# Performance work log

Measured on AMD Instinct MI355X. Metric: run time of the kernel, lower is better.

## Reference

```python
import jax, jax.numpy as jnp
import numpy as np

N, C, G, R = 500000, 256, 1024, 16


def setup_inputs() -> dict:
    key = jax.random.key(0)
    k1, k2, k3, k4 = jax.random.split(key, 4)
    x = jax.random.normal(k1, (N, C), dtype=jnp.float32)
    batch_idx = jnp.sort(jax.random.randint(k2, (N,), 0, G))
    # torch Linear weights: W1 [C//R, C], W2 [C, C//R] (no bias)
    W1 = jax.random.normal(k3, (C // R, C), dtype=jnp.float32) / np.sqrt(C)
    W2 = jax.random.normal(k4, (C, C // R), dtype=jnp.float32) / np.sqrt(C // R)
    prelu_a = jnp.asarray(0.25, dtype=jnp.float32)  # nn.PReLU default single param
    return {"x": x, "batch_idx": batch_idx, "num_graphs": G,
            "W1": W1, "prelu_a": prelu_a, "W2": W2}


def reference(x, batch_idx, num_graphs, W1, prelu_a, W2):
    # scatter_mean over graphs: [G, C]
    seg_sum = jax.ops.segment_sum(x, batch_idx, num_segments=num_graphs)
    cnt = jax.ops.segment_sum(jnp.ones((x.shape[0],), x.dtype), batch_idx,
                              num_segments=num_graphs)
    x_mean = seg_sum / jnp.maximum(cnt, 1.0)[:, None]
    # SE bottleneck MLP: Linear -> PReLU -> Linear -> Sigmoid
    h = jnp.einsum('gc,rc->gr', x_mean, W1)          # [G, C//R]
    h = jnp.where(h >= 0, h, prelu_a * h)            # PReLU (scalar a)
    score = jax.nn.sigmoid(jnp.einsum('gr,cr->gc', h, W2))  # [G, C]
    # gather-broadcast multiply back to nodes
    return x * score[batch_idx]
```

## Files before the change

kernel.cpp:

```cpp
#include <hip/hip_runtime.h>

#define CC 256
#define GG 1024
#define RR 16
#define ROWS_PER_BLOCK 256

__global__ void seg_sum_kernel(const float* __restrict__ x,
                               const int* __restrict__ batch_idx,
                               float* __restrict__ seg,
                               float* __restrict__ cnt,
                               int n) {
    const int wave = threadIdx.x >> 6;
    const int lane = threadIdx.x & 63;
    const int base = blockIdx.x * ROWS_PER_BLOCK;
    const int rend = min(base + ROWS_PER_BLOCK, n);

    float4 acc = make_float4(0.f, 0.f, 0.f, 0.f);
    int cur_g = -1;
    int cl = 0;

    for (int row = base + wave; row < rend; row += 4) {
        const int g = batch_idx[row];
        if (g != cur_g) {
            if (cur_g >= 0) {
                float* p = seg + (size_t)cur_g * CC + lane * 4;
                atomicAdd(p + 0, acc.x);
                atomicAdd(p + 1, acc.y);
                atomicAdd(p + 2, acc.z);
                atomicAdd(p + 3, acc.w);
                if (lane == 0) atomicAdd(cnt + cur_g, (float)cl);
            }
            cur_g = g;
            acc = make_float4(0.f, 0.f, 0.f, 0.f);
            cl = 0;
        }
        const float4 v =
            *reinterpret_cast<const float4*>(x + (size_t)row * CC + lane * 4);
        acc.x += v.x; acc.y += v.y; acc.z += v.z; acc.w += v.w;
        ++cl;
    }
    if (cur_g >= 0) {
        float* p = seg + (size_t)cur_g * CC + lane * 4;
        atomicAdd(p + 0, acc.x);
        atomicAdd(p + 1, acc.y);
        atomicAdd(p + 2, acc.z);
        atomicAdd(p + 3, acc.w);
        if (lane == 0) atomicAdd(cnt + cur_g, (float)cl);
    }
}

__global__ void mlp_kernel(const float* __restrict__ seg,
                           const float* __restrict__ cnt,
                           const float* __restrict__ W1,
                           const float* __restrict__ prelu_a,
                           const float* __restrict__ W2,
                           float* __restrict__ score) {
    __shared__ float xm[CC];
    __shared__ float h[RR];
    const int g = blockIdx.x;
    const int t = threadIdx.x;

    const float c   = cnt[g];
    const float inv = 1.0f / fmaxf(c, 1.0f);
    xm[t] = seg[(size_t)g * CC + t] * inv;
    __syncthreads();

    if (t < RR) {
        const float a = *prelu_a;
        float acc = 0.f;
        const float* w = W1 + t * CC;
        #pragma unroll 8
        for (int cc2 = 0; cc2 < CC; ++cc2) acc += xm[cc2] * w[cc2];
        h[t] = (acc >= 0.f) ? acc : a * acc;
    }
    __syncthreads();

    float acc2 = 0.f;
    const float* w2 = W2 + t * RR;
    #pragma unroll
    for (int r = 0; r < RR; ++r) acc2 += h[r] * w2[r];
    score[(size_t)g * CC + t] = 1.0f / (1.0f + __expf(-acc2));
}

__global__ void apply_kernel(const float4* __restrict__ x4,
                             const int* __restrict__ batch_idx,
                             const float4* __restrict__ score4,
                             float4* __restrict__ out4,
                             long total) {
    const long i = (long)blockIdx.x * blockDim.x + threadIdx.x;
    if (i >= total) return;
    const int row = (int)(i >> 6);
    const int c4  = (int)(i & 63);
    const int g   = batch_idx[row];
    const float4 v = x4[i];
    const float4 s = score4[(size_t)g * 64 + c4];
    out4[i] = make_float4(v.x * s.x, v.y * s.y, v.z * s.z, v.w * s.w);
}

extern "C" void kernel_launch(void* const* d_in, const int* in_sizes, int n_in,
                              void* d_out, int out_size, void* d_ws, size_t ws_size,
                              hipStream_t stream) {
    const float* x    = (const float*)d_in[0];
    const int*   bidx = (const int*)d_in[1];
    const float* W1   = (const float*)d_in[3];
    const float* pa   = (const float*)d_in[4];
    const float* W2   = (const float*)d_in[5];
    float*       out  = (float*)d_out;

    const int n = in_sizes[1];

    float* seg   = (float*)d_ws;
    float* cnt   = seg + (size_t)GG * CC;
    float* score = cnt + GG;

    hipMemsetAsync(d_ws, 0, ((size_t)GG * CC + GG) * sizeof(float), stream);

    const int nb1 = (n + ROWS_PER_BLOCK - 1) / ROWS_PER_BLOCK;
    seg_sum_kernel<<<nb1, 256, 0, stream>>>(x, bidx, seg, cnt, n);

    mlp_kernel<<<GG, CC, 0, stream>>>(seg, cnt, W1, pa, W2, score);

    const long total = (long)n * (CC / 4);
    const int nb3 = (int)((total + 255) / 256);
    apply_kernel<<<nb3, 256, 0, stream>>>((const float4*)x, bidx,
                                          (const float4*)score, (float4*)out,
                                          total);
}
```

Baseline: 934.5 us.

## Fuse segment mean, SE MLP and scaling into one per-graph kernel

Replaces the atomic segment-sum, MLP and apply kernels with a binary-search bounds kernel plus one fused kernel where each 1024-thread block owns whole graphs. The block reduces the graph's rows in shared memory, computes the MLP score locally, then re-reads the rows to write the scaled output with nontemporal stores. This removes the memset, the atomics, the per-element batch_idx gather and the score round-trip through global memory. In exchange x is read twice inside one block, possibly hitting cache, and only 256 blocks iterate over 1024 graphs, so uneven graph sizes can leave some blocks working longer than others.

```diff
diff --git a/kernel.cpp b/kernel.cpp
--- a/kernel.cpp
+++ b/kernel.cpp
@@ -3,98 +3,103 @@
 #define CC 256
 #define GG 1024
 #define RR 16
-#define ROWS_PER_BLOCK 256
+#define NB 256
+#define NT_THREADS 1024
 
-__global__ void seg_sum_kernel(const float* __restrict__ x,
-                               const int* __restrict__ batch_idx,
-                               float* __restrict__ seg,
-                               float* __restrict__ cnt,
-                               int n) {
-    const int wave = threadIdx.x >> 6;
-    const int lane = threadIdx.x & 63;
-    const int base = blockIdx.x * ROWS_PER_BLOCK;
-    const int rend = min(base + ROWS_PER_BLOCK, n);
+typedef float f32x4 __attribute__((ext_vector_type(4)));
 
-    float4 acc = make_float4(0.f, 0.f, 0.f, 0.f);
-    int cur_g = -1;
-    int cl = 0;
-
-    for (int row = base + wave; row < rend; row += 4) {
-        const int g = batch_idx[row];
-        if (g != cur_g) {
-            if (cur_g >= 0) {
-                float* p = seg + (size_t)cur_g * CC + lane * 4;
-                atomicAdd(p + 0, acc.x);
-                atomicAdd(p + 1, acc.y);
-                atomicAdd(p + 2, acc.z);
-                atomicAdd(p + 3, acc.w);
-                if (lane == 0) atomicAdd(cnt + cur_g, (float)cl);
-            }
-            cur_g = g;
-            acc = make_float4(0.f, 0.f, 0.f, 0.f);
-            cl = 0;
-        }
-        const float4 v =
-            *reinterpret_cast<const float4*>(x + (size_t)row * CC + lane * 4);
-        acc.x += v.x; acc.y += v.y; acc.z += v.z; acc.w += v.w;
-        ++cl;
+__global__ void bounds_kernel(const int* __restrict__ bidx,
+                              int* __restrict__ bounds, int n) {
+    const int g = blockIdx.x * blockDim.x + threadIdx.x;
+    if (g > GG) return;
+    int lo = 0, hi = n;
+    while (lo < hi) {
+        const int mid = (lo + hi) >> 1;
+        if (bidx[mid] < g) lo = mid + 1; else hi = mid;
     }
-    if (cur_g >= 0) {
-        float* p = seg + (size_t)cur_g * CC + lane * 4;
-        atomicAdd(p + 0, acc.x);
-        atomicAdd(p + 1, acc.y);
-        atomicAdd(p + 2, acc.z);
-        atomicAdd(p + 3, acc.w);
-        if (lane == 0) atomicAdd(cnt + cur_g, (float)cl);
-    }
+    bounds[g] = lo;
 }
 
-__global__ void mlp_kernel(const float* __restrict__ seg,
-                           const float* __restrict__ cnt,
-                           const float* __restrict__ W1,
-                           const float* __restrict__ prelu_a,
-                           const float* __restrict__ W2,
-                           float* __restrict__ score) {
+__global__ __launch_bounds__(NT_THREADS) void fused_kernel(
+        const float* __restrict__ x,
+        const int* __restrict__ bounds,
+        const float* __restrict__ W1,
+        const float* __restrict__ prelu_a,
+        const float* __restrict__ W2,
+        float* __restrict__ out) {
+    __shared__ f32x4 part[16][64];
     __shared__ float xm[CC];
     __shared__ float h[RR];
-    const int g = blockIdx.x;
-    const int t = threadIdx.x;
+    __shared__ float score[CC];
 
-    const float c   = cnt[g];
-    const float inv = 1.0f / fmaxf(c, 1.0f);
-    xm[t] = seg[(size_t)g * CC + t] * inv;
-    __syncthreads();
+    const int t    = threadIdx.x;
+    const int w    = t >> 6;
+    const int lane = t & 63;
 
-    if (t < RR) {
-        const float a = *prelu_a;
-        float acc = 0.f;
-        const float* w = W1 + t * CC;
-        #pragma unroll 8
-        for (int cc2 = 0; cc2 < CC; ++cc2) acc += xm[cc2] * w[cc2];
-        h[t] = (acc >= 0.f) ? acc : a * acc;
+    for (int g = blockIdx.x; g < GG; g += gridDim.x) {
+        const int start = bounds[g];
+        const int end   = bounds[g + 1];
+        const int rows  = end - start;
+        if (rows == 0) continue;
+
+        f32x4 acc = {0.f, 0.f, 0.f, 0.f};
+        #pragma unroll 2
+        for (int r = start + w; r < end; r += 16) {
+            const f32x4 v = *reinterpret_cast<const f32x4*>(
+                x + (size_t)r * CC + 4 * lane);
+            acc += v;
+        }
+        part[w][lane] = acc;
+        __syncthreads();
+        if (w < 8) { part[w][lane] += part[w + 8][lane]; } __syncthreads();
+        if (w < 4) { part[w][lane] += part[w + 4][lane]; } __syncthreads();
+        if (w < 2) { part[w][lane] += part[w + 2][lane]; } __syncthreads();
+        if (w == 0) {
+            const float inv = 1.0f / (float)rows;
+            f32x4 s = part[0][lane] + part[1][lane];
+            s *= inv;
+            reinterpret_cast<f32x4*>(xm)[lane] = s;
+        }
+        __syncthreads();
+
+        if (t < 256) {
+            const int r  = t >> 4;
+            const int sl = t & 15;
+            const float* wrow = W1 + r * CC;
+            float p = 0.f;
+            #pragma unroll
+            for (int c = sl; c < CC; c += 16) p += xm[c] * wrow[c];
+            p += __shfl_xor(p, 1);
+            p += __shfl_xor(p, 2);
+            p += __shfl_xor(p, 4);
+            p += __shfl_xor(p, 8);
+            if (sl == 0) {
+                const float a = *prelu_a;
+                h[r] = (p >= 0.f) ? p : a * p;
+            }
+        }
+        __syncthreads();
+
+        if (t < 256) {
+            const float* w2 = W2 + t * RR;
+            float acc2 = 0.f;
+            #pragma unroll
+            for (int r = 0; r < RR; ++r) acc2 += h[r] * w2[r];
+            score[t] = 1.0f / (1.0f + __expf(-acc2));
+        }
+        __syncthreads();
+
+        const f32x4 sv = reinterpret_cast<const f32x4*>(score)[lane];
+        #pragma unroll 2
+        for (int r = start + w; r < end; r += 16) {
+            const f32x4 v = *reinterpret_cast<const f32x4*>(
+                x + (size_t)r * CC + 4 * lane);
+            const f32x4 o = v * sv;
+            __builtin_nontemporal_store(
+                o, reinterpret_cast<f32x4*>(out + (size_t)r * CC + 4 * lane));
+        }
+        __syncthreads();
     }
-    __syncthreads();
-
-    float acc2 = 0.f;
-    const float* w2 = W2 + t * RR;
-    #pragma unroll
-    for (int r = 0; r < RR; ++r) acc2 += h[r] * w2[r];
-    score[(size_t)g * CC + t] = 1.0f / (1.0f + __expf(-acc2));
-}
-
-__global__ void apply_kernel(const float4* __restrict__ x4,
-                             const int* __restrict__ batch_idx,
-                             const float4* __restrict__ score4,
-                             float4* __restrict__ out4,
-                             long total) {
-    const long i = (long)blockIdx.x * blockDim.x + threadIdx.x;
-    if (i >= total) return;
-    const int row = (int)(i >> 6);
-    const int c4  = (int)(i & 63);
-    const int g   = batch_idx[row];
-    const float4 v = x4[i];
-    const float4 s = score4[(size_t)g * 64 + c4];
-    out4[i] = make_float4(v.x * s.x, v.y * s.y, v.z * s.z, v.w * s.w);
 }
 
 extern "C" void kernel_launch(void* const* d_in, const int* in_sizes, int n_in,
@@ -109,20 +114,9 @@
 
     const int n = in_sizes[1];
 
-    float* seg   = (float*)d_ws;
-    float* cnt   = seg + (size_t)GG * CC;
-    float* score = cnt + GG;
+    int* bounds = (int*)d_ws;
 
-    hipMemsetAsync(d_ws, 0, ((size_t)GG * CC + GG) * sizeof(float), stream);
+    bounds_kernel<<<(GG + 1 + 255) / 256, 256, 0, stream>>>(bidx, bounds, n);
 
-    const int nb1 = (n + ROWS_PER_BLOCK - 1) / ROWS_PER_BLOCK;
-    seg_sum_kernel<<<nb1, 256, 0, stream>>>(x, bidx, seg, cnt, n);
-
-    mlp_kernel<<<GG, CC, 0, stream>>>(seg, cnt, W1, pa, W2, score);
-
-    const long total = (long)n * (CC / 4);
-    const int nb3 = (int)((total + 255) / 256);
-    apply_kernel<<<nb3, 256, 0, stream>>>((const float4*)x, bidx,
-                                          (const float4*)score, (float4*)out,
-                                          total);
+    fused_kernel<<<NB, NT_THREADS, 0, stream>>>(x, bounds, W1, pa, W2, out);
 }
```

Result: faster. 878.1 us (-6.0%).
